# Performance work log

Hardware: AMD Instinct MI355X
Metric: run time of the kernel (lower is better)

The kernel has to match this reference:

```python
import jax, jax.numpy as jnp
import numpy as np

NUM_NODES = 100000
NUM_EDGES = 1600000
NUM_GRAPHS = 1000
NUM_FEATURES = 128
DIM = 32
NUM_CLASSES = 10


def setup_inputs() -> dict:
    key = jax.random.key(0)
    ks = jax.random.split(key, 20)
    inp = {
        "x": jax.random.normal(ks[0], (NUM_NODES, NUM_FEATURES), dtype=jnp.float32),
        "edge_index": jax.random.randint(ks[1], (2, NUM_EDGES), 0, NUM_NODES, dtype=jnp.int64),
        "batch": jnp.sort(jax.random.randint(ks[2], (NUM_NODES,), 0, NUM_GRAPHS, dtype=jnp.int64)),
        "edge_weight": jax.random.uniform(ks[3], (NUM_EDGES,), dtype=jnp.float32),
    }
    # GraphConv params: lin_rel (with bias) on aggregated msgs, lin_root (no bias) on x
    dims = [(NUM_FEATURES, DIM)] + [(DIM, DIM)] * 4
    for i, (fi, fo) in enumerate(dims, start=1):
        s = 1.0 / np.sqrt(fi)
        inp[f"Wrel{i}"] = jax.random.uniform(ks[3 + i], (fi, fo), jnp.float32, -s, s)
        inp[f"brel{i}"] = jax.random.uniform(ks[8 + i], (fo,), jnp.float32, -s, s)
        inp[f"Wroot{i}"] = jax.random.uniform(ks[13 + i], (fi, fo), jnp.float32, -s, s)
    s = 1.0 / np.sqrt(DIM)
    inp["Wlin1"] = jax.random.uniform(ks[19], (DIM, DIM), jnp.float32, -s, s)
    inp["blin1"] = jax.random.uniform(jax.random.fold_in(key, 100), (DIM,), jnp.float32, -s, s)
    inp["Wlin2"] = jax.random.uniform(jax.random.fold_in(key, 101), (DIM, NUM_CLASSES), jnp.float32, -s, s)
    inp["blin2"] = jax.random.uniform(jax.random.fold_in(key, 102), (NUM_CLASSES,), jnp.float32, -s, s)
    return inp


def _graph_conv(x, src, dst, ew, Wrel, brel, Wroot, num_nodes):
    # message: x_j * e_ji ; aggregate (add) at target ; out = lin_rel(agg) + lin_root(x)
    msg = x[src] * ew[:, None]                                   # [E, F_in]
    agg = jax.ops.segment_sum(msg, dst, num_segments=num_nodes)  # [N, F_in]
    return agg @ Wrel + brel + x @ Wroot


def reference(x, edge_index, batch, edge_weight,
              Wrel1, brel1, Wroot1, Wrel2, brel2, Wroot2,
              Wrel3, brel3, Wroot3, Wrel4, brel4, Wroot4,
              Wrel5, brel5, Wroot5, Wlin1, blin1, Wlin2, blin2):
    n = x.shape[0]
    src, dst = edge_index[0], edge_index[1]
    h = jax.nn.relu(_graph_conv(x, src, dst, edge_weight, Wrel1, brel1, Wroot1, n))
    h = jax.nn.relu(_graph_conv(h, src, dst, edge_weight, Wrel2, brel2, Wroot2, n))
    h = jax.nn.relu(_graph_conv(h, src, dst, edge_weight, Wrel3, brel3, Wroot3, n))
    h = jax.nn.relu(_graph_conv(h, src, dst, edge_weight, Wrel4, brel4, Wroot4, n))
    h = jax.nn.relu(_graph_conv(h, src, dst, edge_weight, Wrel5, brel5, Wroot5, n))
    g = jax.ops.segment_sum(h, batch, num_segments=NUM_GRAPHS)   # global_add_pool [G, DIM]
    g = jax.nn.relu(g @ Wlin1 + blin1)
    # dropout p=0.5 is identity in eval mode
    logits = g @ Wlin2 + blin2
    return jax.nn.log_softmax(logits, axis=-1)
```

## Files before the change

kernel.cpp:

```cpp
#include <hip/hip_runtime.h>
#include <stdint.h>

#define NN 100000
#define NE 1600000
#define NG 1000
#define FIN 128
#define DIM 32
#define NC 10

#define NBKT 512
#define NPB 196
#define BCAP 4608
#define RND 2048
#define CURS 16
#define NBINB 782
#define NMM1 1563
#define MM1P1 781
#define MM1P2 782

typedef unsigned int u32;
typedef __attribute__((ext_vector_type(8))) short short8;
typedef __attribute__((ext_vector_type(4))) float floatx4;
typedef __attribute__((ext_vector_type(4))) unsigned int uint4e;

__device__ __forceinline__ ushort f2bf(float f) {
    u32 b = __float_as_uint(f);
    return (ushort)((b + 0x7FFFu + ((b >> 16) & 1u)) >> 16);
}
__device__ __forceinline__ float bf2f(ushort u) {
    return __uint_as_float(((u32)u) << 16);
}

struct SBin {
    uint2  ent[RND];
    ushort bk16[RND];
    int cnt[NBKT]; int basep[NBKT]; int gbase[NBKT]; int wsum[4];
};
struct SCsr {
    int hist[NPB]; int base[NPB]; int wsum[4];
};
struct SMm {
    ushort xs[64 * 136];
};
union SMem1 { SBin b; SMm m; };
union SMem2 { SCsr c; SMm m; };

__global__ __launch_bounds__(256) void k_init(u32* __restrict__ zp, int zn,
        const float* __restrict__ W0r, const float* __restrict__ W0o,
        const float* __restrict__ W1r, const float* __restrict__ W1o,
        const float* __restrict__ W2r, const float* __restrict__ W2o,
        const float* __restrict__ W3r, const float* __restrict__ W3o,
        const float* __restrict__ W4r, const float* __restrict__ W4o,
        ushort* __restrict__ wfrag, ushort* __restrict__ wfrag1) {
    int i = blockIdx.x * 256 + threadIdx.x;
    if (i < zn) zp[i] = 0u;
    int t = threadIdx.x;
    int mat  = t >> 7;
    int nh   = (t >> 6) & 1;
    int lane = t & 63;
    int m = lane & 15;
    int g = lane >> 4;
    if (blockIdx.x < 4) {
        const float* Ws[8] = {W1r, W1o, W2r, W2o, W3r, W3o, W4r, W4o};
        const float* W = Ws[blockIdx.x * 2 + mat];
        ushort* dst = wfrag + (((size_t)blockIdx.x * 4 + mat * 2 + nh) * 64 + lane) * 8;
        #pragma unroll
        for (int j = 0; j < 8; ++j)
            dst[j] = f2bf(W[(g * 8 + j) * DIM + nh * 16 + m]);
    } else if (blockIdx.x < 8) {
        int kc = blockIdx.x - 4;
        const float* W = mat ? W0o : W0r;
        int nt = mat * 2 + nh;
        ushort* dst = wfrag1 + (((size_t)nt * 4 + kc) * 64 + lane) * 8;
        #pragma unroll
        for (int j = 0; j < 8; ++j)
            dst[j] = f2bf(W[(kc * 32 + g * 8 + j) * DIM + nh * 16 + m]);
    }
}

__device__ void bin_body(SMem1& sm, int blk, const int* __restrict__ ei,
        const float* __restrict__ ew, int* __restrict__ cursor,
        uint2* __restrict__ ebuf) {
    int tid = threadIdx.x;
    int lane = tid & 63, wv = tid >> 6;
    int e0 = blk * RND;
    int n  = min(RND, NE - e0);

    for (int i = tid; i < NBKT; i += 256) sm.b.cnt[i] = 0;
    __syncthreads();

    u32 pk[8], wvv[8], bp[8];
    #pragma unroll
    for (int q = 0; q < 8; ++q) {
        int i = tid + q * 256;
        pk[q] = 0; wvv[q] = 0; bp[q] = 0;
        if (i < n) {
            int s = ei[e0 + i];
            int d = ei[NE + e0 + i];
            float w = ew[e0 + i];
            int b = d / NPB;
            int loc = d - b * NPB;
            int p = atomicAdd(&sm.b.cnt[b], 1);
            pk[q] = (u32)s | ((u32)loc << 17);
            wvv[q] = __float_as_uint(w);
            bp[q] = (u32)p | ((u32)b << 16);
        }
    }
    __syncthreads();

    int a  = sm.b.cnt[2 * tid];
    int b2 = sm.b.cnt[2 * tid + 1];
    int s  = a + b2;
    int inc = s;
    #pragma unroll
    for (int d = 1; d < 64; d <<= 1) {
        int u = __shfl_up(inc, d);
        if (lane >= d) inc += u;
    }
    if (lane == 63) sm.b.wsum[wv] = inc;
    __syncthreads();
    int off = 0;
    #pragma unroll
    for (int w2 = 0; w2 < 3; ++w2) off += (w2 < wv) ? sm.b.wsum[w2] : 0;
    int ex = off + inc - s;
    sm.b.basep[2 * tid]     = ex;
    sm.b.basep[2 * tid + 1] = ex + a;
    for (int i = tid; i < NBKT; i += 256)
        if (sm.b.cnt[i] > 0) sm.b.gbase[i] = atomicAdd(&cursor[i * CURS], sm.b.cnt[i]);
    __syncthreads();

    #pragma unroll
    for (int q = 0; q < 8; ++q) {
        int i = tid + q * 256;
        if (i < n) {
            int b = (int)(bp[q] >> 16);
            int p = (int)(bp[q] & 0xFFFFu);
            int pos = sm.b.basep[b] + p;
            sm.b.ent[pos]  = make_uint2(pk[q], wvv[q]);
            sm.b.bk16[pos] = (ushort)b;
        }
    }
    __syncthreads();

    for (int i = tid; i < n; i += 256) {
        int b = (int)sm.b.bk16[i];
        int dsti = sm.b.gbase[b] + (i - sm.b.basep[b]);
        if (dsti < BCAP) ebuf[(size_t)b * BCAP + dsti] = sm.b.ent[i];
    }
}

__device__ void csr_body(SMem2& sm, int bkt, uint2* __restrict__ ebuf,
        const int* __restrict__ cursor, uint2* __restrict__ od) {
    int tid = threadIdx.x;
    int lane = tid & 63, wvx = tid >> 6;
    int cnt = min(cursor[bkt * CURS], 4096);
    for (int i = tid; i < NPB; i += 256) sm.c.hist[i] = 0;
    __syncthreads();
    uint2* gb = ebuf + (size_t)bkt * BCAP;
    uint2 my[16]; int mp[16];
    #pragma unroll
    for (int q = 0; q < 16; ++q) {
        int i = tid + q * 256;
        mp[q] = -1;
        if (i < cnt) {
            my[q] = gb[i];
            int loc = (int)(my[q].x >> 17);
            mp[q] = atomicAdd(&sm.c.hist[loc], 1);
        }
    }
    __syncthreads();
    int h  = (tid < NPB) ? sm.c.hist[tid] : 0;
    int hp = (h + 7) & ~7;
    int inc = hp;
    #pragma unroll
    for (int d = 1; d < 64; d <<= 1) {
        int u = __shfl_up(inc, d);
        if (lane >= d) inc += u;
    }
    if (lane == 63) sm.c.wsum[wvx] = inc;
    __syncthreads();
    int off = 0;
    #pragma unroll
    for (int w2 = 0; w2 < 3; ++w2) off += (w2 < wvx) ? sm.c.wsum[w2] : 0;
    if (tid < NPB) sm.c.base[tid] = off + inc - hp;
    __syncthreads();
    int tot = sm.c.wsum[0] + sm.c.wsum[1] + sm.c.wsum[2] + sm.c.wsum[3];
    tot = min(tot, BCAP);
    for (int i = tid; i < tot; i += 256) gb[i] = make_uint2(0u, 0u);
    __syncthreads();
    #pragma unroll
    for (int q = 0; q < 16; ++q) {
        if (mp[q] >= 0) {
            int loc = (int)(my[q].x >> 17);
            int pos = sm.c.base[loc] + mp[q];
            if (pos < BCAP) gb[pos] = my[q];
        }
    }
    for (int i = tid; i < NPB; i += 256) {
        int node = bkt * NPB + i;
        if (node < NN) {
            int dg = sm.c.hist[i];
            int bs = sm.c.base[i];
            if (bs + ((dg + 7) & ~7) > BCAP) dg = max(0, BCAP - bs) & ~7;
            od[node] = make_uint2((u32)(bkt * BCAP + bs), (u32)dg);
        }
    }
}

__device__ void mm1_body(ushort* __restrict__ xs, int blk, const float* __restrict__ x,
        const ushort* __restrict__ wfrag1, const float* __restrict__ brel,
        ushort* __restrict__ ybf, float* __restrict__ aggi) {
    int tid = threadIdx.x;
    int base = blk * 64;
    for (int i = tid; i < 64 * 32; i += 256) {
        int r = i >> 5, c = i & 31;
        int node = base + r;
        float4 v = make_float4(0.f, 0.f, 0.f, 0.f);
        if (node < NN) v = ((const float4*)x)[(size_t)node * 32 + c];
        ushort4 u;
        u.x = f2bf(v.x); u.y = f2bf(v.y); u.z = f2bf(v.z); u.w = f2bf(v.w);
        *(ushort4*)&xs[r * 136 + c * 4] = u;
    }
    int lane = tid & 63;
    int w = tid >> 6;
    int m = lane & 15;
    int q = lane >> 4;
    short8 bfr[4][4];
    #pragma unroll
    for (int nt = 0; nt < 4; ++nt)
        #pragma unroll
        for (int kc = 0; kc < 4; ++kc)
            bfr[nt][kc] = *(const short8*)&wfrag1[(((size_t)nt * 4 + kc) * 64 + lane) * 8];
    __syncthreads();
    floatx4 acc[4] = {{0.f,0.f,0.f,0.f},{0.f,0.f,0.f,0.f},{0.f,0.f,0.f,0.f},{0.f,0.f,0.f,0.f}};
    #pragma unroll
    for (int kc = 0; kc < 4; ++kc) {
        short8 af = *(const short8*)&xs[(w * 16 + m) * 136 + kc * 32 + q * 8];
        #pragma unroll
        for (int nt = 0; nt < 4; ++nt)
            acc[nt] = __builtin_amdgcn_mfma_f32_16x16x32_bf16(af, bfr[nt][kc], acc[nt], 0, 0, 0);
    }
    float br0 = brel[m], br1 = brel[16 + m];
    #pragma unroll
    for (int reg = 0; reg < 4; ++reg) {
        int row = q * 4 + reg;
        int node = base + w * 16 + row;
        if (node < NN) {
            ybf[(size_t)node * 32 + m]       = f2bf(acc[0][reg]);
            ybf[(size_t)node * 32 + 16 + m]  = f2bf(acc[1][reg]);
            aggi[(size_t)node * 32 + m]      = acc[2][reg] + br0;
            aggi[(size_t)node * 32 + 16 + m] = acc[3][reg] + br1;
        }
    }
}

__global__ __launch_bounds__(256) void k_pre1(const int* __restrict__ ei,
        const float* __restrict__ ew, int* __restrict__ cursor, uint2* __restrict__ ebuf,
        const float* __restrict__ x, const ushort* __restrict__ wfrag1,
        const float* __restrict__ brel,
        ushort* __restrict__ ybf, float* __restrict__ aggi) {
    __shared__ SMem1 sm;
    if (blockIdx.x < NBINB) bin_body(sm, blockIdx.x, ei, ew, cursor, ebuf);
    else                    mm1_body(sm.m.xs, blockIdx.x - NBINB, x, wfrag1, brel, ybf, aggi);
}

__global__ __launch_bounds__(256) void k_pre2(uint2* __restrict__ ebuf,
        const int* __restrict__ cursor, uint2* __restrict__ od,
        const float* __restrict__ x, const ushort* __restrict__ wfrag1,
        const float* __restrict__ brel,
        ushort* __restrict__ ybf, float* __restrict__ aggi) {
    __shared__ SMem2 sm;
    if (blockIdx.x < NBKT) csr_body(sm, blockIdx.x, ebuf, cursor, od);
    else                   mm1_body(sm.m.xs, blockIdx.x - NBKT + MM1P1, x, wfrag1, brel, ybf, aggi);
}

__device__ __forceinline__ float2 gather_accum(const uint2* __restrict__ eb, int deg,
        const uint* __restrict__ ybp) {
    float acc0 = 0.f, acc1 = 0.f;
    int b = 0;
    for (; b + 8 < deg; b += 16) {
        const uint4e* p = (const uint4e*)(eb + b);
        uint4e e0 = __builtin_nontemporal_load(p + 0);
        uint4e e1 = __builtin_nontemporal_load(p + 1);
        uint4e e2 = __builtin_nontemporal_load(p + 2);
        uint4e e3 = __builtin_nontemporal_load(p + 3);
        uint4e e4 = __builtin_nontemporal_load(p + 4);
        uint4e e5 = __builtin_nontemporal_load(p + 5);
        uint4e e6 = __builtin_nontemporal_load(p + 6);
        uint4e e7 = __builtin_nontemporal_load(p + 7);
        uint u0  = ybp[(e0.x & 0x1FFFFu) << 4];
        uint u1  = ybp[(e0.z & 0x1FFFFu) << 4];
        uint u2  = ybp[(e1.x & 0x1FFFFu) << 4];
        uint u3  = ybp[(e1.z & 0x1FFFFu) << 4];
        uint u4  = ybp[(e2.x & 0x1FFFFu) << 4];
        uint u5  = ybp[(e2.z & 0x1FFFFu) << 4];
        uint u6  = ybp[(e3.x & 0x1FFFFu) << 4];
        uint u7  = ybp[(e3.z & 0x1FFFFu) << 4];
        uint u8  = ybp[(e4.x & 0x1FFFFu) << 4];
        uint u9  = ybp[(e4.z & 0x1FFFFu) << 4];
        uint u10 = ybp[(e5.x & 0x1FFFFu) << 4];
        uint u11 = ybp[(e5.z & 0x1FFFFu) << 4];
        uint u12 = ybp[(e6.x & 0x1FFFFu) << 4];
        uint u13 = ybp[(e6.z & 0x1FFFFu) << 4];
        uint u14 = ybp[(e7.x & 0x1FFFFu) << 4];
        uint u15 = ybp[(e7.z & 0x1FFFFu) << 4];
        acc0 += __uint_as_float(e0.y) * __uint_as_float(u0 << 16);
        acc1 += __uint_as_float(e0.y) * __uint_as_float(u0 & 0xFFFF0000u);
        acc0 += __uint_as_float(e0.w) * __uint_as_float(u1 << 16);
        acc1 += __uint_as_float(e0.w) * __uint_as_float(u1 & 0xFFFF0000u);
        acc0 += __uint_as_float(e1.y) * __uint_as_float(u2 << 16);
        acc1 += __uint_as_float(e1.y) * __uint_as_float(u2 & 0xFFFF0000u);
        acc0 += __uint_as_float(e1.w) * __uint_as_float(u3 << 16);
        acc1 += __uint_as_float(e1.w) * __uint_as_float(u3 & 0xFFFF0000u);
        acc0 += __uint_as_float(e2.y) * __uint_as_float(u4 << 16);
        acc1 += __uint_as_float(e2.y) * __uint_as_float(u4 & 0xFFFF0000u);
        acc0 += __uint_as_float(e2.w) * __uint_as_float(u5 << 16);
        acc1 += __uint_as_float(e2.w) * __uint_as_float(u5 & 0xFFFF0000u);
        acc0 += __uint_as_float(e3.y) * __uint_as_float(u6 << 16);
        acc1 += __uint_as_float(e3.y) * __uint_as_float(u6 & 0xFFFF0000u);
        acc0 += __uint_as_float(e3.w) * __uint_as_float(u7 << 16);
        acc1 += __uint_as_float(e3.w) * __uint_as_float(u7 & 0xFFFF0000u);
        acc0 += __uint_as_float(e4.y) * __uint_as_float(u8 << 16);
        acc1 += __uint_as_float(e4.y) * __uint_as_float(u8 & 0xFFFF0000u);
        acc0 += __uint_as_float(e4.w) * __uint_as_float(u9 << 16);
        acc1 += __uint_as_float(e4.w) * __uint_as_float(u9 & 0xFFFF0000u);
        acc0 += __uint_as_float(e5.y) * __uint_as_float(u10 << 16);
        acc1 += __uint_as_float(e5.y) * __uint_as_float(u10 & 0xFFFF0000u);
        acc0 += __uint_as_float(e5.w) * __uint_as_float(u11 << 16);
        acc1 += __uint_as_float(e5.w) * __uint_as_float(u11 & 0xFFFF0000u);
        acc0 += __uint_as_float(e6.y) * __uint_as_float(u12 << 16);
        acc1 += __uint_as_float(e6.y) * __uint_as_float(u12 & 0xFFFF0000u);
        acc0 += __uint_as_float(e6.w) * __uint_as_float(u13 << 16);
        acc1 += __uint_as_float(e6.w) * __uint_as_float(u13 & 0xFFFF0000u);
        acc0 += __uint_as_float(e7.y) * __uint_as_float(u14 << 16);
        acc1 += __uint_as_float(e7.y) * __uint_as_float(u14 & 0xFFFF0000u);
        acc0 += __uint_as_float(e7.w) * __uint_as_float(u15 << 16);
        acc1 += __uint_as_float(e7.w) * __uint_as_float(u15 & 0xFFFF0000u);
    }
    if (b < deg) {
        const uint4e* p = (const uint4e*)(eb + b);
        uint4e e0 = __builtin_nontemporal_load(p + 0);
        uint4e e1 = __builtin_nontemporal_load(p + 1);
        uint4e e2 = __builtin_nontemporal_load(p + 2);
        uint4e e3 = __builtin_nontemporal_load(p + 3);
        uint u0 = ybp[(e0.x & 0x1FFFFu) << 4];
        uint u1 = ybp[(e0.z & 0x1FFFFu) << 4];
        uint u2 = ybp[(e1.x & 0x1FFFFu) << 4];
        uint u3 = ybp[(e1.z & 0x1FFFFu) << 4];
        uint u4 = ybp[(e2.x & 0x1FFFFu) << 4];
        uint u5 = ybp[(e2.z & 0x1FFFFu) << 4];
        uint u6 = ybp[(e3.x & 0x1FFFFu) << 4];
        uint u7 = ybp[(e3.z & 0x1FFFFu) << 4];
        acc0 += __uint_as_float(e0.y) * __uint_as_float(u0 << 16);
        acc1 += __uint_as_float(e0.y) * __uint_as_float(u0 & 0xFFFF0000u);
        acc0 += __uint_as_float(e0.w) * __uint_as_float(u1 << 16);
        acc1 += __uint_as_float(e0.w) * __uint_as_float(u1 & 0xFFFF0000u);
        acc0 += __uint_as_float(e1.y) * __uint_as_float(u2 << 16);
        acc1 += __uint_as_float(e1.y) * __uint_as_float(u2 & 0xFFFF0000u);
        acc0 += __uint_as_float(e1.w) * __uint_as_float(u3 << 16);
        acc1 += __uint_as_float(e1.w) * __uint_as_float(u3 & 0xFFFF0000u);
        acc0 += __uint_as_float(e2.y) * __uint_as_float(u4 << 16);
        acc1 += __uint_as_float(e2.y) * __uint_as_float(u4 & 0xFFFF0000u);
        acc0 += __uint_as_float(e2.w) * __uint_as_float(u5 << 16);
        acc1 += __uint_as_float(e2.w) * __uint_as_float(u5 & 0xFFFF0000u);
        acc0 += __uint_as_float(e3.y) * __uint_as_float(u6 << 16);
        acc1 += __uint_as_float(e3.y) * __uint_as_float(u6 & 0xFFFF0000u);
        acc0 += __uint_as_float(e3.w) * __uint_as_float(u7 << 16);
        acc1 += __uint_as_float(e3.w) * __uint_as_float(u7 & 0xFFFF0000u);
    }
    return make_float2(acc0, acc1);
}

__global__ __launch_bounds__(256, 6) void k_gfused(const ushort* __restrict__ ybf,
        const uint2* __restrict__ ebuf, const uint2* __restrict__ od,
        const float* __restrict__ aggi, const ushort* __restrict__ wfragL,
        const float* __restrict__ brel,
        ushort* __restrict__ ybf_n, float* __restrict__ aggi_n) {
    __shared__ __align__(16) ushort hsm[16 * 40];
    int tid  = threadIdx.x;
    int w    = tid >> 6;
    int lane = tid & 63;
    int nl   = lane >> 4;
    int fp   = lane & 15;
    int node = blockIdx.x * 16 + w * 4 + nl;
    short8 bfr = *(const short8*)&wfragL[((size_t)w * 64 + lane) * 8];
    uint2 o = od[node];
    const uint2* eb = ebuf + o.x;
    const uint* ybp = (const uint*)ybf + fp;
    float2 pv = *(const float2*)&aggi[(size_t)node * DIM + fp * 2];
    float2 ac = gather_accum(eb, (int)o.y, ybp);
    float h0 = fmaxf(pv.x + ac.x, 0.f);
    float h1 = fmaxf(pv.y + ac.y, 0.f);
    u32 hp = (u32)f2bf(h0) | ((u32)f2bf(h1) << 16);
    *(u32*)&hsm[(w * 4 + nl) * 40 + fp * 2] = hp;
    __syncthreads();
    short8 af = *(const short8*)&hsm[(lane & 15) * 40 + (lane >> 4) * 8];
    floatx4 acc = {0.f, 0.f, 0.f, 0.f};
    acc = __builtin_amdgcn_mfma_f32_16x16x32_bf16(af, bfr, acc, 0, 0, 0);
    int ncol  = (w & 1) * 16 + (lane & 15);
    int drow0 = (lane >> 4) * 4;
    size_t obase = ((size_t)blockIdx.x * 16 + drow0) * DIM + ncol;
    if (w < 2) {
        #pragma unroll
        for (int r = 0; r < 4; ++r)
            ybf_n[obase + (size_t)r * DIM] = f2bf(acc[r]);
    } else {
        float bb = brel[ncol];
        #pragma unroll
        for (int r = 0; r < 4; ++r)
            __builtin_nontemporal_store(acc[r] + bb, &aggi_n[obase + (size_t)r * DIM]);
    }
}

__global__ __launch_bounds__(256, 6) void k_glast_pool(const ushort* __restrict__ ybf,
        const uint2* __restrict__ ebuf, const uint2* __restrict__ od,
        const float* __restrict__ aggi, const int* __restrict__ batch,
        float* __restrict__ g) {
    __shared__ __align__(16) float hsm[16][34];
    int tid  = threadIdx.x;
    int w    = tid >> 6;
    int lane = tid & 63;
    int nl   = lane >> 4;
    int fp   = lane & 15;
    int node = blockIdx.x * 16 + w * 4 + nl;
    uint2 o = od[node];
    const uint2* eb = ebuf + o.x;
    const uint* ybp = (const uint*)ybf + fp;
    float2 pv = *(const float2*)&aggi[(size_t)node * DIM + fp * 2];
    float2 ac = gather_accum(eb, (int)o.y, ybp);
    float2 hv;
    hv.x = fmaxf(pv.x + ac.x, 0.f);
    hv.y = fmaxf(pv.y + ac.y, 0.f);
    *(float2*)&hsm[w * 4 + nl][fp * 2] = hv;
    __syncthreads();
    if (tid < 32) {
        int nb = blockIdx.x * 16;
        int curb = batch[nb];
        float run = 0.f;
        #pragma unroll
        for (int n = 0; n < 16; ++n) {
            int b = batch[nb + n];
            if (b != curb) {
                atomicAdd(&g[(size_t)curb * DIM + tid], run);
                run = 0.f; curb = b;
            }
            run += hsm[n][tid];
        }
        atomicAdd(&g[(size_t)curb * DIM + tid], run);
    }
}

__global__ __launch_bounds__(64) void k_head(const float* __restrict__ g,
        const float* __restrict__ W1, const float* __restrict__ b1,
        const float* __restrict__ W2, const float* __restrict__ b2,
        float* __restrict__ out) {
    __shared__ float gs[DIM];
    __shared__ float a1[DIM];
    __shared__ float lg[NC];
    int t = threadIdx.x;
    int gr = blockIdx.x;
    if (t < DIM) gs[t] = g[(size_t)gr * DIM + t];
    __syncthreads();
    if (t < DIM) {
        float a = b1[t];
        #pragma unroll
        for (int k = 0; k < DIM; ++k) a += gs[k] * W1[k * DIM + t];
        a1[t] = fmaxf(a, 0.f);
    }
    __syncthreads();
    if (t < NC) {
        float a = b2[t];
        #pragma unroll
        for (int k = 0; k < DIM; ++k) a += a1[k] * W2[k * NC + t];
        lg[t] = a;
    }
    __syncthreads();
    if (t == 0) {
        float m = lg[0];
        for (int c = 1; c < NC; ++c) m = fmaxf(m, lg[c]);
        float s = 0.f;
        for (int c = 0; c < NC; ++c) s += expf(lg[c] - m);
        float ls = m + logf(s);
        for (int c = 0; c < NC; ++c) out[(size_t)gr * NC + c] = lg[c] - ls;
    }
}

extern "C" void kernel_launch(void* const* d_in, const int* in_sizes, int n_in,
                              void* d_out, int out_size, void* d_ws, size_t ws_size,
                              hipStream_t stream) {
    const float* x     = (const float*)d_in[0];
    const int*   ei    = (const int*)d_in[1];
    const int*   batch = (const int*)d_in[2];
    const float* ew    = (const float*)d_in[3];
    const float* Wrel[5]  = {(const float*)d_in[4],  (const float*)d_in[7],  (const float*)d_in[10], (const float*)d_in[13], (const float*)d_in[16]};
    const float* brel[5]  = {(const float*)d_in[5],  (const float*)d_in[8],  (const float*)d_in[11], (const float*)d_in[14], (const float*)d_in[17]};
    const float* Wroot[5] = {(const float*)d_in[6],  (const float*)d_in[9],  (const float*)d_in[12], (const float*)d_in[15], (const float*)d_in[18]};
    const float* W1 = (const float*)d_in[19];
    const float* b1 = (const float*)d_in[20];
    const float* W2 = (const float*)d_in[21];
    const float* b2 = (const float*)d_in[22];
    float* out = (float*)d_out;

    char* ws = (char*)d_ws;
    const size_t off_cursor = 0;
    const size_t off_g      = 32768;
    const size_t zero_end   = 160768;
    const size_t off_wfrag  = 160768;
    const size_t off_wfrag1 = 177152;
    const size_t off_ebuf   = 193536;
    const size_t ebuf_bytes = ((size_t)NBKT * BCAP + 64) * 8;
    const size_t off_od     = off_ebuf + ebuf_bytes;
    const size_t off_A      = off_od + (size_t)NN * 8;
    const size_t off_C      = off_A + (size_t)NN * DIM * 4;
    const size_t off_B1     = off_C + (size_t)NN * DIM * 4;
    const size_t off_B2     = off_B1 + (size_t)NN * DIM * 2;
    const size_t need       = off_B2 + (size_t)NN * DIM * 2;
    if (ws_size < need) return;

    int*    cursor = (int*)(ws + off_cursor);
    float*  g      = (float*)(ws + off_g);
    ushort* wfrag  = (ushort*)(ws + off_wfrag);
    ushort* wfrag1 = (ushort*)(ws + off_wfrag1);
    uint2*  ebuf   = (uint2*)(ws + off_ebuf);
    uint2*  od     = (uint2*)(ws + off_od);
    float*  A      = (float*)(ws + off_A);
    float*  C      = (float*)(ws + off_C);
    ushort* B1     = (ushort*)(ws + off_B1);
    ushort* B2     = (ushort*)(ws + off_B2);

    int zcount = (int)(zero_end / 4);
    k_init<<<(zcount + 255) / 256, 256, 0, stream>>>((u32*)ws, zcount,
        Wrel[0], Wroot[0], Wrel[1], Wroot[1], Wrel[2], Wroot[2],
        Wrel[3], Wroot[3], Wrel[4], Wroot[4], wfrag, wfrag1);

    k_pre1<<<NBINB + MM1P1, 256, 0, stream>>>(ei, ew, cursor, ebuf,
                                              x, wfrag1, brel[0], B1, A);
    k_pre2<<<NBKT + MM1P2, 256, 0, stream>>>(ebuf, cursor, od,
                                             x, wfrag1, brel[0], B1, A);

    const int ngt = NN / 16;
    float*  aggc = A;  float*  aggn = C;
    ushort* yc   = B1; ushort* yn   = B2;
    for (int L = 1; L < 5; ++L) {
        k_gfused<<<ngt, 256, 0, stream>>>(yc, ebuf, od, aggc,
                                          wfrag + (size_t)(L - 1) * 2048, brel[L], yn, aggn);
        float* tf = aggc; aggc = aggn; aggn = tf;
        ushort* tu = yc; yc = yn; yn = tu;
    }
    k_glast_pool<<<ngt, 256, 0, stream>>>(yc, ebuf, od, aggc, batch, g);
    k_head<<<NG, 64, 0, stream>>>(g, W1, b1, W2, b2, out);
}
```

Baseline: 354.4 us.

## Scatter binned edges directly to global buckets and raise occupancy bounds

The edge-binning pass no longer stages entries in shared memory with a block prefix scan. Each edge is written straight to its global bucket slot from registers, using its per-block atomic offset plus the bucket's global base. Each bin block now handles twice as many edges with half as many blocks, and launch bounds rise to 8 waves per SIMD on several kernels. This removes the LDS staging, scan and extra barriers, but the scattered global writes are less coalesced and the higher occupancy target may cause register spills.

```diff
diff --git a/kernel.cpp b/kernel.cpp
--- a/kernel.cpp
+++ b/kernel.cpp
@@ -11,9 +11,9 @@
 #define NBKT 512
 #define NPB 196
 #define BCAP 4608
-#define RND 2048
+#define RND 4096
 #define CURS 16
-#define NBINB 782
+#define NBINB 391
 #define NMM1 1563
 #define MM1P1 781
 #define MM1P2 782
@@ -32,9 +32,7 @@
 }
 
 struct SBin {
-    uint2  ent[RND];
-    ushort bk16[RND];
-    int cnt[NBKT]; int basep[NBKT]; int gbase[NBKT]; int wsum[4];
+    int cnt[NBKT]; int gbase[NBKT];
 };
 struct SCsr {
     int hist[NPB]; int base[NPB]; int wsum[4];
@@ -82,18 +80,17 @@
         const float* __restrict__ ew, int* __restrict__ cursor,
         uint2* __restrict__ ebuf) {
     int tid = threadIdx.x;
-    int lane = tid & 63, wv = tid >> 6;
     int e0 = blk * RND;
     int n  = min(RND, NE - e0);
 
     for (int i = tid; i < NBKT; i += 256) sm.b.cnt[i] = 0;
     __syncthreads();
 
-    u32 pk[8], wvv[8], bp[8];
-    #pragma unroll
-    for (int q = 0; q < 8; ++q) {
+    u32 pk[16], wvv[16], bp[16];
+    #pragma unroll
+    for (int q = 0; q < 16; ++q) {
         int i = tid + q * 256;
-        pk[q] = 0; wvv[q] = 0; bp[q] = 0;
+        bp[q] = 0xFFFFFFFFu;
         if (i < n) {
             int s = ei[e0 + i];
             int d = ei[NE + e0 + i];
@@ -101,51 +98,27 @@
             int b = d / NPB;
             int loc = d - b * NPB;
             int p = atomicAdd(&sm.b.cnt[b], 1);
-            pk[q] = (u32)s | ((u32)loc << 17);
+            pk[q]  = (u32)s | ((u32)loc << 17);
             wvv[q] = __float_as_uint(w);
-            bp[q] = (u32)p | ((u32)b << 16);
-        }
-    }
-    __syncthreads();
-
-    int a  = sm.b.cnt[2 * tid];
-    int b2 = sm.b.cnt[2 * tid + 1];
-    int s  = a + b2;
-    int inc = s;
-    #pragma unroll
-    for (int d = 1; d < 64; d <<= 1) {
-        int u = __shfl_up(inc, d);
-        if (lane >= d) inc += u;
-    }
-    if (lane == 63) sm.b.wsum[wv] = inc;
-    __syncthreads();
-    int off = 0;
-    #pragma unroll
-    for (int w2 = 0; w2 < 3; ++w2) off += (w2 < wv) ? sm.b.wsum[w2] : 0;
-    int ex = off + inc - s;
-    sm.b.basep[2 * tid]     = ex;
-    sm.b.basep[2 * tid + 1] = ex + a;
-    for (int i = tid; i < NBKT; i += 256)
-        if (sm.b.cnt[i] > 0) sm.b.gbase[i] = atomicAdd(&cursor[i * CURS], sm.b.cnt[i]);
-    __syncthreads();
-
-    #pragma unroll
-    for (int q = 0; q < 8; ++q) {
-        int i = tid + q * 256;
-        if (i < n) {
+            bp[q]  = (u32)p | ((u32)b << 16);
+        }
+    }
+    __syncthreads();
+
+    for (int i = tid; i < NBKT; i += 256) {
+        int c = sm.b.cnt[i];
+        sm.b.gbase[i] = (c > 0) ? atomicAdd(&cursor[i * CURS], c) : 0;
+    }
+    __syncthreads();
+
+    #pragma unroll
+    for (int q = 0; q < 16; ++q) {
+        if (bp[q] != 0xFFFFFFFFu) {
             int b = (int)(bp[q] >> 16);
             int p = (int)(bp[q] & 0xFFFFu);
-            int pos = sm.b.basep[b] + p;
-            sm.b.ent[pos]  = make_uint2(pk[q], wvv[q]);
-            sm.b.bk16[pos] = (ushort)b;
-        }
-    }
-    __syncthreads();
-
-    for (int i = tid; i < n; i += 256) {
-        int b = (int)sm.b.bk16[i];
-        int dsti = sm.b.gbase[b] + (i - sm.b.basep[b]);
-        if (dsti < BCAP) ebuf[(size_t)b * BCAP + dsti] = sm.b.ent[i];
+            int pos = sm.b.gbase[b] + p;
+            if (pos < BCAP) ebuf[(size_t)b * BCAP + pos] = make_uint2(pk[q], wvv[q]);
+        }
     }
 }
 
@@ -254,7 +227,7 @@
     }
 }
 
-__global__ __launch_bounds__(256) void k_pre1(const int* __restrict__ ei,
+__global__ __launch_bounds__(256, 8) void k_pre1(const int* __restrict__ ei,
         const float* __restrict__ ew, int* __restrict__ cursor, uint2* __restrict__ ebuf,
         const float* __restrict__ x, const ushort* __restrict__ wfrag1,
         const float* __restrict__ brel,
@@ -264,7 +237,7 @@
     else                    mm1_body(sm.m.xs, blockIdx.x - NBINB, x, wfrag1, brel, ybf, aggi);
 }
 
-__global__ __launch_bounds__(256) void k_pre2(uint2* __restrict__ ebuf,
+__global__ __launch_bounds__(256, 8) void k_pre2(uint2* __restrict__ ebuf,
         const int* __restrict__ cursor, uint2* __restrict__ od,
         const float* __restrict__ x, const ushort* __restrict__ wfrag1,
         const float* __restrict__ brel,
@@ -371,7 +344,7 @@
     return make_float2(acc0, acc1);
 }
 
-__global__ __launch_bounds__(256, 6) void k_gfused(const ushort* __restrict__ ybf,
+__global__ __launch_bounds__(256, 8) void k_gfused(const ushort* __restrict__ ybf,
         const uint2* __restrict__ ebuf, const uint2* __restrict__ od,
         const float* __restrict__ aggi, const ushort* __restrict__ wfragL,
         const float* __restrict__ brel,
@@ -412,7 +385,7 @@
     }
 }
 
-__global__ __launch_bounds__(256, 6) void k_glast_pool(const ushort* __restrict__ ybf,
+__global__ __launch_bounds__(256, 8) void k_glast_pool(const ushort* __restrict__ ybf,
         const uint2* __restrict__ ebuf, const uint2* __restrict__ od,
         const float* __restrict__ aggi, const int* __restrict__ batch,
         float* __restrict__ g) {
```

Result: slower. 399.3 us (+12.7%).
